# Optimization experiments

Measured on AMD Instinct MI355X. Metric: run time of the kernel, lower is better.

## Reference

```python
import jax, jax.numpy as jnp
import numpy as np

OBS_DIM = 512
ACT_DIM = 32
HIDDEN_DIM = 1024
MSG_DIM = 128
POS_EM_DIM = 128
T = 256


def pos_table(n, dim):
    pos = np.arange(n)[:, None].astype(np.float64)
    j = np.arange(dim)[None, :]
    tab = pos / np.power(10000.0, 2 * (j // 2) / dim)
    tab[:, 0::2] = np.sin(tab[:, 0::2])
    tab[:, 1::2] = np.cos(tab[:, 1::2])
    return tab.astype(np.float32)


def setup_inputs() -> dict:
    key = jax.random.key(0)
    ks = jax.random.split(key, 12)
    in_dim = 1 + ACT_DIM
    s = 0.1
    return {
        "obs": jax.random.normal(ks[0], (T, OBS_DIM), jnp.float32),
        "prev_act": jax.random.normal(ks[1], (T, ACT_DIM), jnp.float32),
        "in_shift": jnp.zeros((OBS_DIM,), jnp.float32),
        "in_scale": jnp.ones((OBS_DIM,), jnp.float32),
        "pos_embedding": jnp.asarray(pos_table(HIDDEN_DIM, POS_EM_DIM)),
        "W_ih": s * jax.random.normal(ks[2], (4 * POS_EM_DIM, in_dim), jnp.float32),
        "b_ih": s * jax.random.normal(ks[3], (4 * POS_EM_DIM,), jnp.float32),
        "W_hh": s * jax.random.normal(ks[4], (4 * POS_EM_DIM, POS_EM_DIM), jnp.float32),
        "b_hh": s * jax.random.normal(ks[5], (4 * POS_EM_DIM,), jnp.float32),
        "Wq": s * jax.random.normal(ks[6], (MSG_DIM, POS_EM_DIM), jnp.float32),
        "bq": s * jax.random.normal(ks[7], (MSG_DIM,), jnp.float32),
        "Wk": s * jax.random.normal(ks[8], (MSG_DIM, POS_EM_DIM), jnp.float32),
        "bk": s * jax.random.normal(ks[9], (MSG_DIM,), jnp.float32),
    }


def reference(obs, prev_act, in_shift, in_scale, pos_embedding,
              W_ih, b_ih, W_hh, b_hh, Wq, bq, Wk, bk):
    # input normalization (buffers default to identity)
    x = (obs - in_shift) / (in_scale + 1e-8)  # (T, obs_dim)
    # query projection of the positional table is constant across steps
    q = pos_embedding @ Wq.T + bq             # (hidden_dim, msg_dim)
    inv_scale = 1.0 / jnp.sqrt(jnp.float32(MSG_DIM))

    def step(carry, inp):
        h, c = carry                            # (obs_dim, pos_em_dim) each
        s, a = inp                              # (obs_dim,), (act_dim,)
        # state-action pair: each obs scalar paired with the full prev action
        xa = jnp.concatenate(
            [s[:, None], jnp.broadcast_to(a, (OBS_DIM, ACT_DIM))], axis=-1)
        gates = xa @ W_ih.T + b_ih + h @ W_hh.T + b_hh
        i, f, g, o = jnp.split(gates, 4, axis=-1)  # torch LSTMCell gate order
        c = jax.nn.sigmoid(f) * c + jax.nn.sigmoid(i) * jnp.tanh(g)
        h = jax.nn.sigmoid(o) * jnp.tanh(c)
        k = h @ Wk.T + bk                       # (obs_dim, msg_dim)
        w = jnp.tanh((q @ k.T) * inv_scale)     # (hidden_dim, obs_dim)
        out = w @ s                             # (hidden_dim,)
        return (h, c), out

    h0 = jnp.zeros((OBS_DIM, POS_EM_DIM), x.dtype)
    c0 = jnp.zeros_like(h0)
    _, outs = jax.lax.scan(step, (h0, c0), (x, prev_act))
    return jnp.tanh(outs)                       # (T, hidden_dim)
```

## Files before the change

kernel.cpp:

```cpp
#include <hip/hip_runtime.h>
#include <hip/hip_fp16.h>

#define T_STEPS 256
#define OBS 512
#define ACT 32
#define HID 1024
#define PED 128
#define MSG 128
#define GATES 512
#define HSTR 136
#define KSTR 17
#define L1 1.4426950408889634f
#define L2C 2.8853900817779268f
#define QSCALE 0.2550348805576823f

typedef _Float16 half8  __attribute__((ext_vector_type(8)));
typedef float    floatx4 __attribute__((ext_vector_type(4)));

__device__ __forceinline__ float fast_exp2(float x) { return __builtin_amdgcn_exp2f(x); }
__device__ __forceinline__ float fast_rcp(float x)  { return __builtin_amdgcn_rcpf(x); }
__device__ __forceinline__ float tanh_f(float x) {
    return fmaf(-2.0f, fast_rcp(fast_exp2(2.8853900817779268f * x) + 1.0f), 1.0f);
}

__global__ void k_pre(const float* __restrict__ obs, const float* __restrict__ act,
                      const float* __restrict__ shift, const float* __restrict__ scale,
                      const float* __restrict__ W_ih, const float* __restrict__ b_ih,
                      const float* __restrict__ b_hh,
                      float* __restrict__ xnorm, float* __restrict__ apre_p) {
    int t = blockIdx.x;
    int tid = threadIdx.x;
    __shared__ float a_s[ACT];
    if (tid < ACT) a_s[tid] = act[t * ACT + tid];
    __syncthreads();
    for (int n = tid; n < OBS; n += 256) {
        xnorm[t * OBS + n] = (obs[t * OBS + n] - shift[n]) / (scale[n] + 1e-8f);
    }
    for (int j = tid; j < GATES; j += 256) {
        float acc = b_ih[j] + b_hh[j];
        const float* wr = W_ih + j * 33 + 1;
#pragma unroll
        for (int u = 0; u < ACT; ++u) acc = fmaf(a_s[u], wr[u], acc);
        int g = j >> 7, p = j & 127;
        apre_p[t * GATES + p * 4 + g] = acc;
    }
}

__global__ void k_qproj(const float* __restrict__ pe, const float* __restrict__ Wq,
                        const float* __restrict__ bq, const float* __restrict__ Wk,
                        const float* __restrict__ bk,
                        _Float16* __restrict__ qh, float* __restrict__ cb) {
    int m = blockIdx.x;
    int d = threadIdx.x;
    __shared__ float pe_s[PED];
    __shared__ float q_s[PED];
    __shared__ float red_s[2];
    pe_s[d] = pe[m * PED + d];
    __syncthreads();
    const float* wr = Wq + d * PED;
    float a = bq[d];
#pragma unroll 8
    for (int p = 0; p < PED; ++p) a = fmaf(pe_s[p], wr[p], a);
    q_s[d] = a;
    float pb = a * bk[d];
#pragma unroll
    for (int off = 32; off; off >>= 1) pb += __shfl_xor(pb, off, 64);
    if ((d & 63) == 0) red_s[d >> 6] = pb;
    __syncthreads();
    float acc = 0.f;
#pragma unroll 8
    for (int p = 0; p < PED; ++p) acc = fmaf(q_s[p], Wk[p * PED + d], acc);
    qh[m * PED + d] = (_Float16)(acc * QSCALE);
    if (d == 0) cb[m] = (red_s[0] + red_s[1]) * QSCALE;
}

__global__ __launch_bounds__(512, 1)
void k_lstm(const float* __restrict__ xnorm, const float* __restrict__ apre_p,
            const float* __restrict__ W_ih, const float* __restrict__ W_hh,
            _Float16* __restrict__ H16) {
    const int tid = threadIdx.x;
    const int lane = tid & 63, wv = tid >> 6;
    const int l15 = lane & 15, quad = lane >> 4;
    const int n0 = blockIdx.x * 4;
    const int p = 16 * wv + l15;

    half8 bfr[4][4];
    float wih0[4];
#pragma unroll
    for (int g = 0; g < 4; ++g) {
        const int col = 128 * g + p;
        const float* wrow = W_hh + (size_t)col * PED;
#pragma unroll
        for (int c = 0; c < 4; ++c) {
            const int k0 = c * 32 + quad * 8;
            float4 f0 = *(const float4*)(wrow + k0);
            float4 f1 = *(const float4*)(wrow + k0 + 4);
            bfr[g][c] = (half8){(_Float16)f0.x, (_Float16)f0.y, (_Float16)f0.z, (_Float16)f0.w,
                                (_Float16)f1.x, (_Float16)f1.y, (_Float16)f1.z, (_Float16)f1.w};
        }
        wih0[g] = W_ih[(size_t)col * 33];
    }

    __shared__ _Float16 h_s[2][16 * HSTR];
    __shared__ float x_s[T_STEPS * 4];

    for (int idx = tid; idx < T_STEPS * 4; idx += 512)
        x_s[idx] = xnorm[(idx >> 2) * OBS + n0 + (idx & 3)];
    for (int idx = tid; idx < 2 * 16 * HSTR; idx += 512)
        ((_Float16*)h_s)[idx] = (_Float16)0.f;

    float c0 = 0.f;
    const float* apl = apre_p + p * 4;
    float4 ap = *(const float4*)(apl);
    __syncthreads();

    _Float16* Hg = H16 + (size_t)(n0 + quad) * MSG + p;
    int buf = 0;
    for (int t = 0; t < T_STEPS; ++t) {
        half8 af[4];
        const _Float16* hb = h_s[buf] + l15 * HSTR + quad * 8;
#pragma unroll
        for (int c = 0; c < 4; ++c) af[c] = *(const half8*)(hb + c * 32);

        floatx4 acc[4];
        acc[0] = (floatx4){ap.x, ap.x, ap.x, ap.x};
        acc[1] = (floatx4){ap.y, ap.y, ap.y, ap.y};
        acc[2] = (floatx4){ap.z, ap.z, ap.z, ap.z};
        acc[3] = (floatx4){ap.w, ap.w, ap.w, ap.w};
#pragma unroll
        for (int g = 0; g < 4; ++g)
#pragma unroll
            for (int c = 0; c < 4; ++c)
                acc[g] = __builtin_amdgcn_mfma_f32_16x16x32_f16(
                    af[c], bfr[g][c], acc[g], 0, 0, 0);

        const int tn = (t + 1 < T_STEPS) ? t + 1 : t;
        float4 ap_n = *(const float4*)(apl + tn * GATES);

        const float x = x_s[t * 4 + quad];
        float gi = fmaf(x, wih0[0], acc[0][0]);
        float gf = fmaf(x, wih0[1], acc[1][0]);
        float gg = fmaf(x, wih0[2], acc[2][0]);
        float go = fmaf(x, wih0[3], acc[3][0]);

        float Di = 1.f + fast_exp2(fminf(-L1 * gi, 20.f));
        float Df = 1.f + fast_exp2(fminf(-L1 * gf, 20.f));
        float Dg = 1.f + fast_exp2(fminf(L2C * gg, 20.f));
        float DfDg = Df * Dg, DiDg = Di * Dg, DiDf = Di * Df;
        float r3 = fast_rcp(Di * DfDg);
        float iDi = r3 * DfDg, iDf = r3 * DiDg, iDg = r3 * DiDf;
        float cn = fmaf(iDf, c0, iDi * fmaf(-2.f, iDg, 1.f));
        c0 = cn;
        float Do = 1.f + fast_exp2(fminf(-L1 * go, 20.f));
        float Dc = 1.f + fast_exp2(fminf(L2C * cn, 20.f));
        float r2 = fast_rcp(Do * Dc);
        float iDo = r2 * Dc, iDc = r2 * Do;
        _Float16 hq = (_Float16)(iDo * fmaf(-2.f, iDc, 1.f));

        h_s[buf ^ 1][(4 * quad) * HSTR + p] = hq;
        Hg[0] = hq;
        Hg += OBS * MSG;

        ap = ap_n;
        buf ^= 1;
        __syncthreads();
    }
}

__global__ __launch_bounds__(256, 4)
void k_attn(const _Float16* __restrict__ qh, const float* __restrict__ cb,
            const _Float16* __restrict__ H16, const float* __restrict__ xnorm,
            float* __restrict__ outp) {
    const int t = blockIdx.x & 255;
    const int mq = blockIdx.x >> 8;
    const int tid = threadIdx.x;
    const int lane = tid & 63, wave = tid >> 6;
    const int l15 = lane & 15, quad = lane >> 4;
    const int m0 = mq * 128 + wave * 32;

    half8 afrag[2][4];
    floatx4 cbv[2];
#pragma unroll
    for (int mt = 0; mt < 2; ++mt) {
        const half8* qrow = (const half8*)(qh + (size_t)(m0 + mt * 16 + l15) * PED);
#pragma unroll
        for (int c = 0; c < 4; ++c) afrag[mt][c] = qrow[c * 4 + quad];
        cbv[mt] = *(const floatx4*)(cb + m0 + mt * 16 + quad * 4);
    }

    __shared__ half8 kbuf[64 * KSTR];
    __shared__ float s_s[64];

    float outacc[8];
#pragma unroll
    for (int i = 0; i < 8; ++i) outacc[i] = 0.f;

    const half8* Ht = (const half8*)(H16 + (size_t)t * (OBS * MSG));
    half8 pf[4];
    float sf = 0.f;
#pragma unroll
    for (int i = 0; i < 4; ++i) pf[i] = Ht[i * 256 + tid];
    if (tid < 64) sf = xnorm[t * OBS + tid];

    for (int ch = 0; ch < 8; ++ch) {
        __syncthreads();
#pragma unroll
        for (int i = 0; i < 4; ++i) {
            int f = i * 256 + tid;
            kbuf[(f >> 4) * KSTR + (f & 15)] = pf[i];
        }
        if (tid < 64) s_s[tid] = sf;
        __syncthreads();
        if (ch < 7) {
            const half8* Hn = Ht + (ch + 1) * 1024;
#pragma unroll
            for (int i = 0; i < 4; ++i) pf[i] = Hn[i * 256 + tid];
            if (tid < 64) sf = xnorm[t * OBS + (ch + 1) * 64 + tid];
        }

#pragma unroll
        for (int nt = 0; nt < 4; ++nt) {
            half8 bfrag[4];
#pragma unroll
            for (int c = 0; c < 4; ++c)
                bfrag[c] = kbuf[(nt * 16 + l15) * KSTR + c * 4 + quad];

            floatx4 acc[2];
#pragma unroll
            for (int mt = 0; mt < 2; ++mt) {
                acc[mt] = cbv[mt];
#pragma unroll
                for (int c = 0; c < 4; ++c)
                    acc[mt] = __builtin_amdgcn_mfma_f32_16x16x32_f16(
                        afrag[mt][c], bfrag[c], acc[mt], 0, 0, 0);
            }

            const float sv = s_s[nt * 16 + l15];
#pragma unroll
            for (int mt = 0; mt < 2; ++mt) {
                float E0 = fast_exp2(fminf(acc[mt][0], 20.f));
                float E1 = fast_exp2(fminf(acc[mt][1], 20.f));
                float E2 = fast_exp2(fminf(acc[mt][2], 20.f));
                float E3 = fast_exp2(fminf(acc[mt][3], 20.f));
                float D0 = 1.f + E0, D1 = 1.f + E1, D2 = 1.f + E2, D3 = 1.f + E3;
                float m01 = D0 * D1, m23 = D2 * D3;
                float rp = fast_rcp(m01 * m23);
                float rA = rp * m23, rB = rp * m01;
                float i0 = rA * D1, i1 = rA * D0, i2 = rB * D3, i3 = rB * D2;
                outacc[mt * 4 + 0] = fmaf(fmaf(-2.f, i0, 1.f), sv, outacc[mt * 4 + 0]);
                outacc[mt * 4 + 1] = fmaf(fmaf(-2.f, i1, 1.f), sv, outacc[mt * 4 + 1]);
                outacc[mt * 4 + 2] = fmaf(fmaf(-2.f, i2, 1.f), sv, outacc[mt * 4 + 2]);
                outacc[mt * 4 + 3] = fmaf(fmaf(-2.f, i3, 1.f), sv, outacc[mt * 4 + 3]);
            }
        }
    }

#pragma unroll
    for (int i = 0; i < 8; ++i) {
        float v = outacc[i];
        v += __shfl_xor(v, 1, 16);
        v += __shfl_xor(v, 2, 16);
        v += __shfl_xor(v, 4, 16);
        v += __shfl_xor(v, 8, 16);
        outacc[i] = v;
    }
    if (l15 == 0) {
        const int mbase = m0 + quad * 4;
#pragma unroll
        for (int mt = 0; mt < 2; ++mt)
#pragma unroll
            for (int r = 0; r < 4; ++r)
                outp[(size_t)t * HID + mbase + mt * 16 + r] = tanh_f(outacc[mt * 4 + r]);
    }
}

extern "C" void kernel_launch(void* const* d_in, const int* in_sizes, int n_in,
                              void* d_out, int out_size, void* d_ws, size_t ws_size,
                              hipStream_t stream) {
    const float* obs      = (const float*)d_in[0];
    const float* prev_act = (const float*)d_in[1];
    const float* in_shift = (const float*)d_in[2];
    const float* in_scale = (const float*)d_in[3];
    const float* pos_emb  = (const float*)d_in[4];
    const float* W_ih     = (const float*)d_in[5];
    const float* b_ih     = (const float*)d_in[6];
    const float* W_hh     = (const float*)d_in[7];
    const float* b_hh     = (const float*)d_in[8];
    const float* Wq       = (const float*)d_in[9];
    const float* bq       = (const float*)d_in[10];
    const float* Wk       = (const float*)d_in[11];
    const float* bk       = (const float*)d_in[12];
    float* outp = (float*)d_out;

    float* ws = (float*)d_ws;
    float* xnorm  = ws;
    float* apre_p = ws + 131072;
    _Float16* qh  = (_Float16*)(ws + 262144);
    float* cbuf   = ws + 327680;
    _Float16* H16 = (_Float16*)(ws + 328704);

    k_pre<<<T_STEPS, 256, 0, stream>>>(obs, prev_act, in_shift, in_scale,
                                       W_ih, b_ih, b_hh, xnorm, apre_p);
    k_qproj<<<HID, 128, 0, stream>>>(pos_emb, Wq, bq, Wk, bk, qh, cbuf);
    k_lstm<<<128, 512, 0, stream>>>(xnorm, apre_p, W_ih, W_hh, H16);
    k_attn<<<T_STEPS * 8, 256, 0, stream>>>(qh, cbuf, H16, xnorm, outp);
}
```

Measured before the change: 300.6 us.

## Batch LSTM gate prefetch and H stores; widen attention tiles with double-buffered K

The LSTM recurrence now prefetches precomputed input gates eight steps at a time into registers and buffers h values so global H writes happen in groups of eight, inside a 16-way unrolled loop. This is meant to keep global load latency off the serial per-step critical path. The attention kernel now has each block cover 256 query rows instead of 128, halving the grid and reusing each K chunk across more MFMAs. It double-buffers K in shared memory with one barrier per chunk and reads the x values directly from global memory. Register pressure rises in both kernels, which may lower occupancy.

```diff
diff --git a/kernel.cpp b/kernel.cpp
--- a/kernel.cpp
+++ b/kernel.cpp
@@ -111,59 +111,83 @@
 
     float c0 = 0.f;
     const float* apl = apre_p + p * 4;
-    float4 ap = *(const float4*)(apl);
-    __syncthreads();
-
-    _Float16* Hg = H16 + (size_t)(n0 + quad) * MSG + p;
-    int buf = 0;
-    for (int t = 0; t < T_STEPS; ++t) {
-        half8 af[4];
-        const _Float16* hb = h_s[buf] + l15 * HSTR + quad * 8;
-#pragma unroll
-        for (int c = 0; c < 4; ++c) af[c] = *(const half8*)(hb + c * 32);
-
-        floatx4 acc[4];
-        acc[0] = (floatx4){ap.x, ap.x, ap.x, ap.x};
-        acc[1] = (floatx4){ap.y, ap.y, ap.y, ap.y};
-        acc[2] = (floatx4){ap.z, ap.z, ap.z, ap.z};
-        acc[3] = (floatx4){ap.w, ap.w, ap.w, ap.w};
-#pragma unroll
-        for (int g = 0; g < 4; ++g)
-#pragma unroll
-            for (int c = 0; c < 4; ++c)
-                acc[g] = __builtin_amdgcn_mfma_f32_16x16x32_f16(
-                    af[c], bfr[g][c], acc[g], 0, 0, 0);
-
-        const int tn = (t + 1 < T_STEPS) ? t + 1 : t;
-        float4 ap_n = *(const float4*)(apl + tn * GATES);
-
-        const float x = x_s[t * 4 + quad];
-        float gi = fmaf(x, wih0[0], acc[0][0]);
-        float gf = fmaf(x, wih0[1], acc[1][0]);
-        float gg = fmaf(x, wih0[2], acc[2][0]);
-        float go = fmaf(x, wih0[3], acc[3][0]);
-
-        float Di = 1.f + fast_exp2(fminf(-L1 * gi, 20.f));
-        float Df = 1.f + fast_exp2(fminf(-L1 * gf, 20.f));
-        float Dg = 1.f + fast_exp2(fminf(L2C * gg, 20.f));
-        float DfDg = Df * Dg, DiDg = Di * Dg, DiDf = Di * Df;
-        float r3 = fast_rcp(Di * DfDg);
-        float iDi = r3 * DfDg, iDf = r3 * DiDg, iDg = r3 * DiDf;
-        float cn = fmaf(iDf, c0, iDi * fmaf(-2.f, iDg, 1.f));
-        c0 = cn;
-        float Do = 1.f + fast_exp2(fminf(-L1 * go, 20.f));
-        float Dc = 1.f + fast_exp2(fminf(L2C * cn, 20.f));
-        float r2 = fast_rcp(Do * Dc);
-        float iDo = r2 * Dc, iDc = r2 * Do;
-        _Float16 hq = (_Float16)(iDo * fmaf(-2.f, iDc, 1.f));
-
-        h_s[buf ^ 1][(4 * quad) * HSTR + p] = hq;
-        Hg[0] = hq;
-        Hg += OBS * MSG;
-
-        ap = ap_n;
-        buf ^= 1;
-        __syncthreads();
+
+    float4 apX[8], apY[8];
+#pragma unroll
+    for (int j = 0; j < 8; ++j) apX[j] = *(const float4*)(apl + (size_t)j * GATES);
+
+    _Float16 hreg[8];
+    _Float16* Hg0 = H16 + (size_t)(n0 + quad) * MSG + p;
+    __syncthreads();
+
+    for (int hg = 0; hg < 16; ++hg) {
+        const int TB = hg * 16;
+#pragma unroll
+        for (int uu = 0; uu < 16; ++uu) {
+            if (uu == 0) {
+                const int tl = TB + 8;
+#pragma unroll
+                for (int j = 0; j < 8; ++j)
+                    apY[j] = *(const float4*)(apl + (size_t)(tl + j) * GATES);
+            }
+            if (uu == 8) {
+                const int tl = (TB + 16) & 255;
+#pragma unroll
+                for (int j = 0; j < 8; ++j)
+                    apX[j] = *(const float4*)(apl + (size_t)(tl + j) * GATES);
+            }
+            const int t = TB + uu;
+            const float4 ap = (uu < 8) ? apX[uu] : apY[uu - 8];
+            const int rb = uu & 1;
+
+            half8 af[4];
+            const _Float16* hb = h_s[rb] + l15 * HSTR + quad * 8;
+#pragma unroll
+            for (int c = 0; c < 4; ++c) af[c] = *(const half8*)(hb + c * 32);
+
+            floatx4 acc[4];
+            acc[0] = (floatx4){ap.x, ap.x, ap.x, ap.x};
+            acc[1] = (floatx4){ap.y, ap.y, ap.y, ap.y};
+            acc[2] = (floatx4){ap.z, ap.z, ap.z, ap.z};
+            acc[3] = (floatx4){ap.w, ap.w, ap.w, ap.w};
+#pragma unroll
+            for (int g = 0; g < 4; ++g)
+#pragma unroll
+                for (int c = 0; c < 4; ++c)
+                    acc[g] = __builtin_amdgcn_mfma_f32_16x16x32_f16(
+                        af[c], bfr[g][c], acc[g], 0, 0, 0);
+
+            const float x = x_s[t * 4 + quad];
+            float gi = fmaf(x, wih0[0], acc[0][0]);
+            float gf = fmaf(x, wih0[1], acc[1][0]);
+            float gg = fmaf(x, wih0[2], acc[2][0]);
+            float go = fmaf(x, wih0[3], acc[3][0]);
+
+            float Di = 1.f + fast_exp2(fminf(-L1 * gi, 20.f));
+            float Df = 1.f + fast_exp2(fminf(-L1 * gf, 20.f));
+            float Dg = 1.f + fast_exp2(fminf(L2C * gg, 20.f));
+            float DfDg = Df * Dg, DiDg = Di * Dg, DiDf = Di * Df;
+            float r3 = fast_rcp(Di * DfDg);
+            float iDi = r3 * DfDg, iDf = r3 * DiDg, iDg = r3 * DiDf;
+            float cn = fmaf(iDf, c0, iDi * fmaf(-2.f, iDg, 1.f));
+            c0 = cn;
+            float Do = 1.f + fast_exp2(fminf(-L1 * go, 20.f));
+            float Dc = 1.f + fast_exp2(fminf(L2C * cn, 20.f));
+            float r2 = fast_rcp(Do * Dc);
+            float iDo = r2 * Dc, iDc = r2 * Do;
+            _Float16 hq = (_Float16)(iDo * fmaf(-2.f, iDc, 1.f));
+
+            h_s[rb ^ 1][(4 * quad) * HSTR + p] = hq;
+            hreg[uu & 7] = hq;
+
+            if ((uu & 7) == 7) {
+                const int tb = t - 7;
+#pragma unroll
+                for (int j = 0; j < 8; ++j)
+                    Hg0[(size_t)(tb + j) * (OBS * MSG)] = hreg[j];
+            }
+            __syncthreads();
+        }
     }
 }
 
@@ -176,46 +200,43 @@
     const int tid = threadIdx.x;
     const int lane = tid & 63, wave = tid >> 6;
     const int l15 = lane & 15, quad = lane >> 4;
-    const int m0 = mq * 128 + wave * 32;
-
-    half8 afrag[2][4];
-    floatx4 cbv[2];
-#pragma unroll
-    for (int mt = 0; mt < 2; ++mt) {
+    const int m0 = mq * 256 + wave * 64;
+
+    half8 afrag[4][4];
+    floatx4 cbv[4];
+#pragma unroll
+    for (int mt = 0; mt < 4; ++mt) {
         const half8* qrow = (const half8*)(qh + (size_t)(m0 + mt * 16 + l15) * PED);
 #pragma unroll
         for (int c = 0; c < 4; ++c) afrag[mt][c] = qrow[c * 4 + quad];
         cbv[mt] = *(const floatx4*)(cb + m0 + mt * 16 + quad * 4);
     }
 
-    __shared__ half8 kbuf[64 * KSTR];
-    __shared__ float s_s[64];
-
-    float outacc[8];
-#pragma unroll
-    for (int i = 0; i < 8; ++i) outacc[i] = 0.f;
+    __shared__ half8 kbuf[2][64 * KSTR];
+
+    float outacc[16];
+#pragma unroll
+    for (int i = 0; i < 16; ++i) outacc[i] = 0.f;
 
     const half8* Ht = (const half8*)(H16 + (size_t)t * (OBS * MSG));
+    const float* xb = xnorm + t * OBS;
+
     half8 pf[4];
-    float sf = 0.f;
 #pragma unroll
     for (int i = 0; i < 4; ++i) pf[i] = Ht[i * 256 + tid];
-    if (tid < 64) sf = xnorm[t * OBS + tid];
+#pragma unroll
+    for (int i = 0; i < 4; ++i) {
+        int f = i * 256 + tid;
+        kbuf[0][(f >> 4) * KSTR + (f & 15)] = pf[i];
+    }
+    __syncthreads();
 
     for (int ch = 0; ch < 8; ++ch) {
-        __syncthreads();
-#pragma unroll
-        for (int i = 0; i < 4; ++i) {
-            int f = i * 256 + tid;
-            kbuf[(f >> 4) * KSTR + (f & 15)] = pf[i];
-        }
-        if (tid < 64) s_s[tid] = sf;
-        __syncthreads();
+        const int cur = ch & 1;
         if (ch < 7) {
             const half8* Hn = Ht + (ch + 1) * 1024;
 #pragma unroll
             for (int i = 0; i < 4; ++i) pf[i] = Hn[i * 256 + tid];
-            if (tid < 64) sf = xnorm[t * OBS + (ch + 1) * 64 + tid];
         }
 
 #pragma unroll
@@ -223,11 +244,11 @@
             half8 bfrag[4];
 #pragma unroll
             for (int c = 0; c < 4; ++c)
-                bfrag[c] = kbuf[(nt * 16 + l15) * KSTR + c * 4 + quad];
-
-            floatx4 acc[2];
-#pragma unroll
-            for (int mt = 0; mt < 2; ++mt) {
+                bfrag[c] = kbuf[cur][(nt * 16 + l15) * KSTR + c * 4 + quad];
+
+            floatx4 acc[4];
+#pragma unroll
+            for (int mt = 0; mt < 4; ++mt) {
                 acc[mt] = cbv[mt];
 #pragma unroll
                 for (int c = 0; c < 4; ++c)
@@ -235,9 +256,9 @@
                         afrag[mt][c], bfrag[c], acc[mt], 0, 0, 0);
             }
 
-            const float sv = s_s[nt * 16 + l15];
-#pragma unroll
-            for (int mt = 0; mt < 2; ++mt) {
+            const float sv = xb[ch * 64 + nt * 16 + l15];
+#pragma unroll
+            for (int mt = 0; mt < 4; ++mt) {
                 float E0 = fast_exp2(fminf(acc[mt][0], 20.f));
                 float E1 = fast_exp2(fminf(acc[mt][1], 20.f));
                 float E2 = fast_exp2(fminf(acc[mt][2], 20.f));
@@ -253,10 +274,19 @@
                 outacc[mt * 4 + 3] = fmaf(fmaf(-2.f, i3, 1.f), sv, outacc[mt * 4 + 3]);
             }
         }
-    }
-
-#pragma unroll
-    for (int i = 0; i < 8; ++i) {
+
+        if (ch < 7) {
+#pragma unroll
+            for (int i = 0; i < 4; ++i) {
+                int f = i * 256 + tid;
+                kbuf[cur ^ 1][(f >> 4) * KSTR + (f & 15)] = pf[i];
+            }
+        }
+        __syncthreads();
+    }
+
+#pragma unroll
+    for (int i = 0; i < 16; ++i) {
         float v = outacc[i];
         v += __shfl_xor(v, 1, 16);
         v += __shfl_xor(v, 2, 16);
@@ -267,7 +297,7 @@
     if (l15 == 0) {
         const int mbase = m0 + quad * 4;
 #pragma unroll
-        for (int mt = 0; mt < 2; ++mt)
+        for (int mt = 0; mt < 4; ++mt)
 #pragma unroll
             for (int r = 0; r < 4; ++r)
                 outp[(size_t)t * HID + mbase + mt * 16 + r] = tanh_f(outacc[mt * 4 + r]);
@@ -303,5 +333,5 @@
                                        W_ih, b_ih, b_hh, xnorm, apre_p);
     k_qproj<<<HID, 128, 0, stream>>>(pos_emb, Wq, bq, Wk, bk, qh, cbuf);
     k_lstm<<<128, 512, 0, stream>>>(xnorm, apre_p, W_ih, W_hh, H16);
-    k_attn<<<T_STEPS * 8, 256, 0, stream>>>(qh, cbuf, H16, xnorm, outp);
-}
+    k_attn<<<T_STEPS * 4, 256, 0, stream>>>(qh, cbuf, H16, xnorm, outp);
+}
```

Result: slower. 387.0 us (+28.7%).
